# Kernel tuning notes

Hardware: AMD Instinct MI355X
Metric: run time of the kernel (lower is better)

The kernel has to match this reference:

```python
import jax, jax.numpy as jnp
import numpy as np
from jax import lax

B, C, H, W = 8, 1024, 64, 48
A = 9  # anchors per location

def _conv(x, w, b, pad):
    y = lax.conv_general_dilated(x, w, (1, 1), pad,
                                 dimension_numbers=('NCHW', 'OIHW', 'NCHW'))
    return y + b[None, :, None, None]

def setup_inputs() -> dict:
    key = jax.random.key(0)
    ks = jax.random.split(key, 12)
    base_feat = jax.random.normal(ks[0], (B, C, H, W), dtype=jnp.float32)
    W_conv = jax.random.normal(ks[1], (512, C, 3, 3), dtype=jnp.float32) * 0.01
    b_conv = jnp.zeros((512,), jnp.float32)
    W_cls = jax.random.normal(ks[2], (18, 512, 1, 1), dtype=jnp.float32) * 0.01
    b_cls = jnp.zeros((18,), jnp.float32)
    W_bbox = jax.random.normal(ks[3], (36, 512, 1, 1), dtype=jnp.float32) * 0.01
    b_bbox = jnp.zeros((36,), jnp.float32)
    # anchor-target-layer outputs (data-dependent assignment) provided as inputs
    rpn_label = (jax.random.randint(ks[4], (B, A * H * W), 0, 3) - 1).astype(jnp.int32)  # {-1,0,1}
    rpn_bbox_targets = jax.random.normal(ks[5], (B, 36, H, W), dtype=jnp.float32) * 0.1
    rpn_bbox_inside_weights = (jax.random.uniform(ks[6], (B, 36, H, W)) < 0.25).astype(jnp.float32)
    rpn_bbox_outside_weights = jax.random.uniform(ks[7], (B, 36, H, W), dtype=jnp.float32) * 0.01
    return {"base_feat": base_feat, "W_conv": W_conv, "b_conv": b_conv,
            "W_cls": W_cls, "b_cls": b_cls, "W_bbox": W_bbox, "b_bbox": b_bbox,
            "rpn_label": rpn_label, "rpn_bbox_targets": rpn_bbox_targets,
            "rpn_bbox_inside_weights": rpn_bbox_inside_weights,
            "rpn_bbox_outside_weights": rpn_bbox_outside_weights}

def reference(base_feat, W_conv, b_conv, W_cls, b_cls, W_bbox, b_bbox,
              rpn_label, rpn_bbox_targets, rpn_bbox_inside_weights,
              rpn_bbox_outside_weights):
    # RPN head: 3x3 conv + relu, then 1x1 cls / bbox heads
    rpn_conv1 = jax.nn.relu(_conv(base_feat, W_conv, b_conv, ((1, 1), (1, 1))))
    cls_score = _conv(rpn_conv1, W_cls, b_cls, ((0, 0), (0, 0)))   # [B,18,H,W]
    bbox_pred = _conv(rpn_conv1, W_bbox, b_bbox, ((0, 0), (0, 0)))  # [B,36,H,W]
    # reshape to [B,2,A*H,W], softmax over the 2-way fg/bg axis, reshape back
    score_rs = cls_score.reshape(B, 2, A * H, W)
    prob_rs = jax.nn.softmax(score_rs, axis=1)
    rpn_cls_prob = prob_rs.reshape(B, 18, H, W)
    # classification loss: permute(0,2,3,1).view(-1,2), keep labels != -1
    logits = score_rs.transpose(0, 2, 3, 1).reshape(-1, 2)
    label = rpn_label.reshape(-1)
    valid = (label != -1).astype(logits.dtype)
    logp = jax.nn.log_softmax(logits, axis=-1)
    lbl = jnp.clip(label, 0, 1)
    nll = -jnp.take_along_axis(logp, lbl[:, None].astype(jnp.int32), axis=1)[:, 0]
    rpn_loss_cls = jnp.sum(nll * valid) / jnp.maximum(jnp.sum(valid), 1.0)
    # smooth-L1 box loss, sigma=3, summed over dims [1,2,3], mean over batch
    sigma2 = 9.0
    in_diff = rpn_bbox_inside_weights * (bbox_pred - rpn_bbox_targets)
    abs_d = jnp.abs(in_diff)
    sign = lax.stop_gradient((abs_d < 1.0 / sigma2).astype(abs_d.dtype))
    in_loss = in_diff * in_diff * (sigma2 / 2.0) * sign + (abs_d - 0.5 / sigma2) * (1.0 - sign)
    rpn_loss_box = jnp.mean(jnp.sum(rpn_bbox_outside_weights * in_loss, axis=(1, 2, 3)))
    return rpn_cls_prob, bbox_pred, rpn_loss_cls, rpn_loss_box
```

## Files before the change

### kernel.cpp

```cpp
#include <hip/hip_runtime.h>
#include <stdint.h>

#define B_    8
#define CIN   1024
#define H_    64
#define W_    48
#define OC    512
#define HW    3072
#define NPOS  24576
#define K9    9216
#define HP    66
#define WP    50

typedef __attribute__((ext_vector_type(8))) __bf16 bf16x8;
typedef __attribute__((ext_vector_type(4))) float  float4_t;
typedef __attribute__((ext_vector_type(4))) unsigned short ushort4_t;
typedef __attribute__((ext_vector_type(8))) int int8v;
typedef __attribute__((ext_vector_type(4))) int int4v;

__device__ __forceinline__ unsigned short f2bf(float x) {
  union { float f; unsigned u; } v; v.f = x;
  unsigned r = v.u + 0x7FFFu + ((v.u >> 16) & 1u);
  return (unsigned short)(r >> 16);
}

__device__ __forceinline__ unsigned int pack4_fp8(float a, float b, float c, float d) {
  int w = __builtin_amdgcn_cvt_pk_fp8_f32(a, b, 0, false);
  w = __builtin_amdgcn_cvt_pk_fp8_f32(c, d, w, true);
  return (unsigned int)w;
}

__device__ __forceinline__ void async16(const void* g, void* l) {
  __builtin_amdgcn_global_load_lds(
      (const __attribute__((address_space(1))) unsigned int*)g,
      (__attribute__((address_space(3))) unsigned int*)l, 16, 0, 0);
}

__device__ __forceinline__ float wave_sum(float v) {
  for (int o = 32; o > 0; o >>= 1) v += __shfl_down(v, o, 64);
  return v;
}

__global__ void prep_fused(const float* __restrict__ x, const float* __restrict__ Wc,
                           const float* __restrict__ Wcls, const float* __restrict__ Wbb,
                           unsigned char* __restrict__ xt, unsigned char* __restrict__ Wa,
                           unsigned short* __restrict__ Wh, float* __restrict__ accbuf) {
  __shared__ float smem[9216];
  int bid = blockIdx.x, t = threadIdx.x;
  if (bid < 4096) {
    int cx = bid & 7, h = (bid >> 3) & 63, b = bid >> 9;
    float* tile = smem;
    const float* src = x + ((long)(b * CIN + cx * 128) * H_ + h) * W_;
    for (int it = 0; it < 6; ++it) {
      int e = it * 256 + t;
      int cl = e / 12, w4 = e % 12;
      float4_t v = *(const float4_t*)&src[(long)cl * HW + w4 * 4];
      int base = cl * 49 + w4 * 4;
      tile[base] = v.x; tile[base + 1] = v.y; tile[base + 2] = v.z; tile[base + 3] = v.w;
    }
    __syncthreads();
    unsigned char* dst = xt + ((long)(b * HP + h + 1) * WP + 1) * CIN + cx * 128;
    for (int it = 0; it < 6; ++it) {
      int e = it * 256 + t;
      int w = e >> 5, g = e & 31;
      float v0 = tile[(g * 4 + 0) * 49 + w] * 16.f;
      float v1 = tile[(g * 4 + 1) * 49 + w] * 16.f;
      float v2 = tile[(g * 4 + 2) * 49 + w] * 16.f;
      float v3 = tile[(g * 4 + 3) * 49 + w] * 16.f;
      *(unsigned int*)&dst[(long)w * CIN + g * 4] = pack4_fp8(v0, v1, v2, v3);
    }
  } else if (bid < 4608) {
    int o = bid - 4096;
    float* lw = smem;
    const float* src = Wc + (long)o * K9;
    for (int i = 0; i < 9; ++i)
      *(float4_t*)&lw[i * 1024 + t * 4] = *(const float4_t*)&src[i * 1024 + t * 4];
    __syncthreads();
    unsigned char* dst = Wa + (long)o * K9;
    int c = t * 4;
    for (int off = 0; off < 9; ++off) {
      float v0 = lw[(c + 0) * 9 + off] * 512.f;
      float v1 = lw[(c + 1) * 9 + off] * 512.f;
      float v2 = lw[(c + 2) * 9 + off] * 512.f;
      float v3 = lw[(c + 3) * 9 + off] * 512.f;
      *(unsigned int*)&dst[off * 1024 + c] = pack4_fp8(v0, v1, v2, v3);
    }
  } else if (bid < 4640) {
    int e = (bid - 4608) * 1024 + t * 4;
    int m = e >> 9, c = e & 511;
    float v0 = 0.f, v1 = 0.f, v2 = 0.f, v3 = 0.f;
    if (m < 18) {
      const float* s = Wcls + m * 512 + c;
      v0 = s[0]; v1 = s[1]; v2 = s[2]; v3 = s[3];
    } else if (m < 54) {
      const float* s = Wbb + (m - 18) * 512 + c;
      v0 = s[0]; v1 = s[1]; v2 = s[2]; v3 = s[3];
    }
    ushort4_t pk; pk.x = f2bf(v0); pk.y = f2bf(v1); pk.z = f2bf(v2); pk.w = f2bf(v3);
    *(ushort4_t*)&Wh[e] = pk;
    if (bid == 4608 && t < 4) accbuf[t] = 0.f;
  } else {
    int bid2 = bid - 4640;
    int b = bid2 / 66, h = bid2 % 66;
    unsigned char* base = xt + (long)(b * 66 + h) * 50 * 1024;
    int4v z = {};
    if (h == 0 || h == 65) {
      for (int i = t; i < 3200; i += 256) *(int4v*)(base + (long)i * 16) = z;
    } else if (t < 128) {
      int which = t >> 6, off = t & 63;
      *(int4v*)(base + (long)which * 49 * 1024 + (long)off * 16) = z;
    }
  }
}

__global__ __launch_bounds__(256, 2)
void conv_gemm(const unsigned char* __restrict__ Wa, const unsigned char* __restrict__ xt,
               const float* __restrict__ bias, unsigned short* __restrict__ conv1) {
  __shared__ unsigned char As_[128 * 128];
  __shared__ unsigned char Bs_[2][192 * 128];
  int t = threadIdx.x;
  int lane = t & 63, wv = t >> 6;
  int m0 = blockIdx.y * 128;
  int n0 = blockIdx.x * 192;
  const unsigned char* aSrc[4];
  const unsigned char* bSrc[6];
  for (int s = 0; s < 4; ++s) {
    int c = s * 256 + t;
    int r = c >> 3;
    int q = (c & 7) ^ (r & 7);
    aSrc[s] = Wa + (long)(m0 + r) * K9 + q * 16;
  }
  for (int p = 0; p < 6; ++p) {
    int c = p * 256 + t;
    int r = c >> 3;
    int q = (c & 7) ^ (r & 7);
    int n = n0 + r; int b = n / HW; int rem = n % HW; int h = rem / W_; int w = rem % W_;
    bSrc[p] = xt + ((long)(b * HP + h) * WP + w) * CIN + q * 16;
  }
  float4_t acc[4][6] = {};
  int wm = wv >> 1, wn = wv & 1;
  int quad = lane >> 4, col = lane & 15;

  auto stageA = [&](int kt) {
    long aoff = (long)kt * 128;
    for (int s = 0; s < 4; ++s)
      async16(aSrc[s] + aoff, &As_[s * 4096 + wv * 1024]);
  };
  auto stageB = [&](int buf, int kt) {
    int off = kt >> 3;
    int dy = off / 3, dx = off % 3;
    long boff = (long)(dy * WP + dx) * CIN + (kt & 7) * 128;
    for (int p = 0; p < 6; ++p)
      async16(bSrc[p] + boff, &Bs_[buf][p * 4096 + wv * 1024]);
  };

  stageA(0);
  stageB(0, 0);
#pragma unroll 1
  for (int kt = 0; kt < 72; ++kt) {
    if (kt + 1 < 72) {
      stageB((kt + 1) & 1, kt + 1);
      asm volatile("s_waitcnt vmcnt(6)\n\ts_barrier" ::: "memory");
    } else {
      asm volatile("s_waitcnt vmcnt(0)\n\ts_barrier" ::: "memory");
    }
    const unsigned char* Bcur = Bs_[kt & 1];
    int8v af[4], bfr[6];
    for (int i = 0; i < 4; ++i) {
      int r = wm * 64 + i * 16 + col;
      int rb = r * 128, x7 = r & 7;
      int4v lo = *(const int4v*)&As_[rb + (((quad * 2 + 0) ^ x7) << 4)];
      int4v hi = *(const int4v*)&As_[rb + (((quad * 2 + 1) ^ x7) << 4)];
      af[i] = (int8v){lo.x, lo.y, lo.z, lo.w, hi.x, hi.y, hi.z, hi.w};
    }
    for (int j = 0; j < 6; ++j) {
      int r = wn * 96 + j * 16 + col;
      int rb = r * 128, x7 = r & 7;
      int4v lo = *(const int4v*)&Bcur[rb + (((quad * 2 + 0) ^ x7) << 4)];
      int4v hi = *(const int4v*)&Bcur[rb + (((quad * 2 + 1) ^ x7) << 4)];
      bfr[j] = (int8v){lo.x, lo.y, lo.z, lo.w, hi.x, hi.y, hi.z, hi.w};
    }
    asm volatile("s_waitcnt lgkmcnt(0)\n\ts_barrier" ::: "memory");
    __builtin_amdgcn_sched_barrier(0);
    if (kt + 1 < 72) stageA(kt + 1);
    __builtin_amdgcn_sched_barrier(0);
    __builtin_amdgcn_s_setprio(1);
    for (int i = 0; i < 4; ++i)
      for (int j = 0; j < 6; ++j)
        acc[i][j] = __builtin_amdgcn_mfma_scale_f32_16x16x128_f8f6f4(
            af[i], bfr[j], acc[i][j], 0, 0, 0, 0x76767676, 0, 0x7B7B7B7B);
    __builtin_amdgcn_s_setprio(0);
    __builtin_amdgcn_sched_barrier(0);
  }

  for (int i = 0; i < 4; ++i) {
    int mb = m0 + wm * 64 + i * 16 + quad * 4;
    float b0 = bias[mb + 0], b1 = bias[mb + 1], b2 = bias[mb + 2], b3 = bias[mb + 3];
    for (int j = 0; j < 6; ++j) {
      int n = n0 + wn * 96 + j * 16 + col;
      ushort4_t pk;
      pk.x = f2bf(fmaxf(acc[i][j].x + b0, 0.f));
      pk.y = f2bf(fmaxf(acc[i][j].y + b1, 0.f));
      pk.z = f2bf(fmaxf(acc[i][j].z + b2, 0.f));
      pk.w = f2bf(fmaxf(acc[i][j].w + b3, 0.f));
      *(ushort4_t*)&conv1[(long)n * 512 + mb] = pk;
    }
  }
}

__global__ __launch_bounds__(256, 2)
void head_gemm(const unsigned short* __restrict__ Wh, const unsigned short* __restrict__ conv1,
               const float* __restrict__ b_cls, const float* __restrict__ b_bbox,
               float* __restrict__ cls_ws, float* __restrict__ out_bbox) {
  __shared__ unsigned short As[64 * 128];
  __shared__ unsigned short Bs[64 * 128];
  int t = threadIdx.x;
  int lane = t & 63, wv = t >> 6;
  int n0 = blockIdx.x * 64;
  int quad = lane >> 4, col = lane & 15;
  const unsigned short* aS[4];
  const unsigned short* bS[4];
  for (int p = 0; p < 4; ++p) {
    int c = p * 256 + t;
    int r = c >> 4;
    int q = (c & 15) ^ (r & 15);
    aS[p] = Wh + (long)r * 512 + q * 8;
    bS[p] = conv1 + (long)(n0 + r) * 512 + q * 8;
  }
  float4_t acc[4] = {};
  for (int kt = 0; kt < 4; ++kt) {
    long koff = (long)kt * 128;
    __syncthreads();
    for (int p = 0; p < 4; ++p) async16(aS[p] + koff, &As[p * 2048 + wv * 512]);
    for (int p = 0; p < 4; ++p) async16(bS[p] + koff, &Bs[p * 2048 + wv * 512]);
    __syncthreads();
    for (int ks = 0; ks < 4; ++ks) {
      int rn = wv * 16 + col;
      bf16x8 bfr = *(const bf16x8*)&Bs[rn * 128 + (((ks * 4 + quad) ^ (rn & 15)) << 3)];
      for (int i = 0; i < 4; ++i) {
        int r = i * 16 + col;
        bf16x8 af = *(const bf16x8*)&As[r * 128 + (((ks * 4 + quad) ^ (r & 15)) << 3)];
        acc[i] = __builtin_amdgcn_mfma_f32_16x16x32_bf16(af, bfr, acc[i], 0, 0, 0);
      }
    }
  }
  int n = n0 + wv * 16 + col;
  int b = n / HW; int rem = n % HW;
  for (int i = 0; i < 4; ++i) {
    for (int r = 0; r < 4; ++r) {
      int m = i * 16 + quad * 4 + r;
      float v = acc[i][r];
      if (m < 18) {
        cls_ws[(long)(b * 18 + m) * HW + rem] = v + b_cls[m];
      } else if (m < 54) {
        out_bbox[(long)(b * 36 + (m - 18)) * HW + rem] = v + b_bbox[m - 18];
      }
    }
  }
}

__global__ void loss_fused(const float* __restrict__ cls, const int* __restrict__ label,
                           float* __restrict__ prob,
                           const float* __restrict__ pred, const float* __restrict__ tgt,
                           const float* __restrict__ iw, const float* __restrict__ ow,
                           float* __restrict__ acc) {
  int lane = threadIdx.x & 63, wv = threadIdx.x >> 6;
  __shared__ float red[8];
  if (blockIdx.x < 864) {
    int idx = blockIdx.x * 256 + threadIdx.x;
    int b = idx / 27648; int r = idx % 27648;
    int a = r / HW; int r2 = r % HW;
    long i0 = (long)(b * 18 + a) * HW + r2;
    long i1 = i0 + (long)9 * HW;
    float x0 = cls[i0], x1 = cls[i1];
    float mx = fmaxf(x0, x1);
    float e0 = __expf(x0 - mx), e1 = __expf(x1 - mx);
    float s = e0 + e1;
    prob[i0] = e0 / s;
    prob[i1] = e1 / s;
    int lb = label[idx];
    float nll = 0.f, val = 0.f;
    if (lb != -1) {
      val = 1.f;
      float xl = (lb > 0) ? x1 : x0;
      nll = -(xl - mx - __logf(s));
    }
    nll = wave_sum(nll);
    val = wave_sum(val);
    if (lane == 0) { red[wv] = nll; red[4 + wv] = val; }
    __syncthreads();
    if (threadIdx.x == 0) {
      atomicAdd(&acc[0], red[0] + red[1] + red[2] + red[3]);
      atomicAdd(&acc[1], red[4] + red[5] + red[6] + red[7]);
    }
  } else {
    int bid = blockIdx.x - 864;
    float s = 0.f;
    const long total = (long)B_ * 36 * HW;
    for (long i = (long)bid * 256 + threadIdx.x; i < total; i += (long)1728 * 256) {
      float d = iw[i] * (pred[i] - tgt[i]);
      float ad = fabsf(d);
      float l = (ad < (1.f / 9.f)) ? d * d * 4.5f : ad - (1.f / 18.f);
      s += ow[i] * l;
    }
    s = wave_sum(s);
    if (lane == 0) red[wv] = s;
    __syncthreads();
    if (threadIdx.x == 0) atomicAdd(&acc[2], red[0] + red[1] + red[2] + red[3]);
  }
}

__global__ void finalize(const float* __restrict__ acc, float* __restrict__ out) {
  if (threadIdx.x == 0) {
    out[0] = acc[0] / fmaxf(acc[1], 1.f);
    out[1] = acc[2] / (float)B_;
  }
}

extern "C" void kernel_launch(void* const* d_in, const int* in_sizes, int n_in,
                              void* d_out, int out_size, void* d_ws, size_t ws_size,
                              hipStream_t stream) {
  const float* base_feat = (const float*)d_in[0];
  const float* W_conv    = (const float*)d_in[1];
  const float* b_conv    = (const float*)d_in[2];
  const float* W_cls     = (const float*)d_in[3];
  const float* b_cls     = (const float*)d_in[4];
  const float* W_bbox    = (const float*)d_in[5];
  const float* b_bbox    = (const float*)d_in[6];
  const int*   rpn_label = (const int*)d_in[7];
  const float* bb_tgt    = (const float*)d_in[8];
  const float* bb_iw     = (const float*)d_in[9];
  const float* bb_ow     = (const float*)d_in[10];

  float* out = (float*)d_out;
  float* out_cls_prob = out;
  float* out_bbox     = out + 442368;
  float* out_scalars  = out + 442368 + 884736;

  size_t off = 0;
  auto alloc = [&](size_t bytes) {
    void* p = (char*)d_ws + off;
    off = (off + bytes + 255) & ~(size_t)255;
    return p;
  };
  const size_t XT_BYTES = (size_t)B_ * HP * WP * CIN;
  unsigned char*  xt    = (unsigned char*)alloc(XT_BYTES);
  unsigned char*  Wa    = (unsigned char*)alloc((size_t)OC * K9);
  unsigned short* conv1 = (unsigned short*)alloc((size_t)NPOS * OC * 2);
  unsigned short* Wh    = (unsigned short*)alloc((size_t)64 * 512 * 2);
  float* cls_ws         = (float*)alloc((size_t)B_ * 18 * HW * 4);
  float* accbuf         = (float*)alloc(16);

  prep_fused<<<5168, 256, 0, stream>>>(base_feat, W_conv, W_cls, W_bbox, xt, Wa, Wh, accbuf);
  conv_gemm<<<dim3(128, 4), 256, 0, stream>>>(Wa, xt, b_conv, conv1);
  head_gemm<<<384, 256, 0, stream>>>(Wh, conv1, b_cls, b_bbox, cls_ws, out_bbox);
  loss_fused<<<2592, 256, 0, stream>>>(cls_ws, rpn_label, out_cls_prob,
                                       out_bbox, bb_tgt, bb_iw, bb_ow, accbuf);
  finalize<<<1, 64, 0, stream>>>(accbuf, out_scalars);
}
```

Measured before the change: 342.5 us.

## Load GEMM A-operand fragments directly from global into registers, dropping LDS staging

```diff
diff --git a/kernel.cpp b/kernel.cpp
--- a/kernel.cpp
+++ b/kernel.cpp
@@ -116,20 +116,14 @@
 __global__ __launch_bounds__(256, 2)
 void conv_gemm(const unsigned char* __restrict__ Wa, const unsigned char* __restrict__ xt,
                const float* __restrict__ bias, unsigned short* __restrict__ conv1) {
-  __shared__ unsigned char As_[128 * 128];
   __shared__ unsigned char Bs_[2][192 * 128];
   int t = threadIdx.x;
   int lane = t & 63, wv = t >> 6;
   int m0 = blockIdx.y * 128;
   int n0 = blockIdx.x * 192;
-  const unsigned char* aSrc[4];
+  int wm = wv >> 1, wn = wv & 1;
+  int quad = lane >> 4, col = lane & 15;
   const unsigned char* bSrc[6];
-  for (int s = 0; s < 4; ++s) {
-    int c = s * 256 + t;
-    int r = c >> 3;
-    int q = (c & 7) ^ (r & 7);
-    aSrc[s] = Wa + (long)(m0 + r) * K9 + q * 16;
-  }
   for (int p = 0; p < 6; ++p) {
     int c = p * 256 + t;
     int r = c >> 3;
@@ -137,15 +131,12 @@
     int n = n0 + r; int b = n / HW; int rem = n % HW; int h = rem / W_; int w = rem % W_;
     bSrc[p] = xt + ((long)(b * HP + h) * WP + w) * CIN + q * 16;
   }
+  const unsigned char* aBase[4];
+  for (int i = 0; i < 4; ++i)
+    aBase[i] = Wa + (long)(m0 + wm * 64 + i * 16 + col) * K9 + quad * 32;
+
   float4_t acc[4][6] = {};
-  int wm = wv >> 1, wn = wv & 1;
-  int quad = lane >> 4, col = lane & 15;
-
-  auto stageA = [&](int kt) {
-    long aoff = (long)kt * 128;
-    for (int s = 0; s < 4; ++s)
-      async16(aSrc[s] + aoff, &As_[s * 4096 + wv * 1024]);
-  };
+
   auto stageB = [&](int buf, int kt) {
     int off = kt >> 3;
     int dy = off / 3, dx = off % 3;
@@ -154,25 +145,26 @@
       async16(bSrc[p] + boff, &Bs_[buf][p * 4096 + wv * 1024]);
   };
 
-  stageA(0);
   stageB(0, 0);
+  __builtin_amdgcn_sched_barrier(0);
+  int4v aLo[4], aHi[4];
+  for (int i = 0; i < 4; ++i) {
+    aLo[i] = *(const int4v*)(aBase[i]);
+    aHi[i] = *(const int4v*)(aBase[i] + 16);
+  }
+  __builtin_amdgcn_sched_barrier(0);
+
 #pragma unroll 1
   for (int kt = 0; kt < 72; ++kt) {
     if (kt + 1 < 72) {
       stageB((kt + 1) & 1, kt + 1);
-      asm volatile("s_waitcnt vmcnt(6)\n\ts_barrier" ::: "memory");
+      asm volatile("s_waitcnt vmcnt(14)\n\ts_barrier" ::: "memory");
     } else {
-      asm volatile("s_waitcnt vmcnt(0)\n\ts_barrier" ::: "memory");
-    }
+      asm volatile("s_waitcnt vmcnt(8)\n\ts_barrier" ::: "memory");
+    }
+    __builtin_amdgcn_sched_barrier(0);
     const unsigned char* Bcur = Bs_[kt & 1];
-    int8v af[4], bfr[6];
-    for (int i = 0; i < 4; ++i) {
-      int r = wm * 64 + i * 16 + col;
-      int rb = r * 128, x7 = r & 7;
-      int4v lo = *(const int4v*)&As_[rb + (((quad * 2 + 0) ^ x7) << 4)];
-      int4v hi = *(const int4v*)&As_[rb + (((quad * 2 + 1) ^ x7) << 4)];
-      af[i] = (int8v){lo.x, lo.y, lo.z, lo.w, hi.x, hi.y, hi.z, hi.w};
-    }
+    int8v bfr[6];
     for (int j = 0; j < 6; ++j) {
       int r = wn * 96 + j * 16 + col;
       int rb = r * 128, x7 = r & 7;
@@ -182,7 +174,15 @@
     }
     asm volatile("s_waitcnt lgkmcnt(0)\n\ts_barrier" ::: "memory");
     __builtin_amdgcn_sched_barrier(0);
-    if (kt + 1 < 72) stageA(kt + 1);
+    int8v af[4];
+    for (int i = 0; i < 4; ++i)
+      af[i] = (int8v){aLo[i].x, aLo[i].y, aLo[i].z, aLo[i].w,
+                      aHi[i].x, aHi[i].y, aHi[i].z, aHi[i].w};
+    long ko = (kt + 1 < 72) ? (long)(kt + 1) * 128 : 0;
+    for (int i = 0; i < 4; ++i) {
+      aLo[i] = *(const int4v*)(aBase[i] + ko);
+      aHi[i] = *(const int4v*)(aBase[i] + ko + 16);
+    }
     __builtin_amdgcn_sched_barrier(0);
     __builtin_amdgcn_s_setprio(1);
     for (int i = 0; i < 4; ++i)
```

Result: slower. 408.1 us (+19.1%).

## Enlarge conv GEMM tile to 256x192 with 8 waves and interleaved A staging

Applied to the files above, without the earlier changes.

```diff
diff --git a/kernel.cpp b/kernel.cpp
--- a/kernel.cpp
+++ b/kernel.cpp
@@ -113,84 +113,125 @@
   }
 }
 
-__global__ __launch_bounds__(256, 2)
+__global__ __launch_bounds__(512, 2)
 void conv_gemm(const unsigned char* __restrict__ Wa, const unsigned char* __restrict__ xt,
                const float* __restrict__ bias, unsigned short* __restrict__ conv1) {
-  __shared__ unsigned char As_[128 * 128];
+  __shared__ unsigned char As_[2][256 * 128];
   __shared__ unsigned char Bs_[2][192 * 128];
   int t = threadIdx.x;
   int lane = t & 63, wv = t >> 6;
-  int m0 = blockIdx.y * 128;
+  int m0 = blockIdx.y * 256;
   int n0 = blockIdx.x * 192;
+  int wm = wv >> 1, wn = wv & 1;
+  int quad = lane >> 4, col = lane & 15;
+
   const unsigned char* aSrc[4];
-  const unsigned char* bSrc[6];
   for (int s = 0; s < 4; ++s) {
-    int c = s * 256 + t;
+    int c = s * 512 + t;
     int r = c >> 3;
     int q = (c & 7) ^ (r & 7);
     aSrc[s] = Wa + (long)(m0 + r) * K9 + q * 16;
   }
-  for (int p = 0; p < 6; ++p) {
-    int c = p * 256 + t;
+  const unsigned char* bSrc[3];
+  for (int p = 0; p < 3; ++p) {
+    int c = p * 512 + t;
     int r = c >> 3;
     int q = (c & 7) ^ (r & 7);
     int n = n0 + r; int b = n / HW; int rem = n % HW; int h = rem / W_; int w = rem % W_;
     bSrc[p] = xt + ((long)(b * HP + h) * WP + w) * CIN + q * 16;
   }
+
   float4_t acc[4][6] = {};
-  int wm = wv >> 1, wn = wv & 1;
-  int quad = lane >> 4, col = lane & 15;
-
-  auto stageA = [&](int kt) {
-    long aoff = (long)kt * 128;
-    for (int s = 0; s < 4; ++s)
-      async16(aSrc[s] + aoff, &As_[s * 4096 + wv * 1024]);
-  };
+
   auto stageB = [&](int buf, int kt) {
     int off = kt >> 3;
     int dy = off / 3, dx = off % 3;
     long boff = (long)(dy * WP + dx) * CIN + (kt & 7) * 128;
-    for (int p = 0; p < 6; ++p)
-      async16(bSrc[p] + boff, &Bs_[buf][p * 4096 + wv * 1024]);
+    for (int p = 0; p < 3; ++p)
+      async16(bSrc[p] + boff, &Bs_[buf][p * 8192 + t * 16]);
   };
-
-  stageA(0);
+  auto stageA2 = [&](int buf, int kt, int s0) {
+    long aoff = (long)kt * 128;
+    for (int s = s0; s < s0 + 2; ++s)
+      async16(aSrc[s] + aoff, &As_[buf][s * 8192 + t * 16]);
+  };
+
   stageB(0, 0);
+  stageA2(0, 0, 0);
+  stageA2(0, 0, 2);
+
 #pragma unroll 1
   for (int kt = 0; kt < 72; ++kt) {
-    if (kt + 1 < 72) {
-      stageB((kt + 1) & 1, kt + 1);
-      asm volatile("s_waitcnt vmcnt(6)\n\ts_barrier" ::: "memory");
+    int cur = kt & 1, nxt = cur ^ 1;
+    if (kt < 71) {
+      stageB(nxt, kt + 1);
+      asm volatile("s_waitcnt vmcnt(3)\n\ts_barrier" ::: "memory");
     } else {
       asm volatile("s_waitcnt vmcnt(0)\n\ts_barrier" ::: "memory");
     }
-    const unsigned char* Bcur = Bs_[kt & 1];
+    const unsigned char* A  = As_[cur];
+    const unsigned char* Bc = Bs_[cur];
     int8v af[4], bfr[6];
     for (int i = 0; i < 4; ++i) {
       int r = wm * 64 + i * 16 + col;
       int rb = r * 128, x7 = r & 7;
-      int4v lo = *(const int4v*)&As_[rb + (((quad * 2 + 0) ^ x7) << 4)];
-      int4v hi = *(const int4v*)&As_[rb + (((quad * 2 + 1) ^ x7) << 4)];
+      int4v lo = *(const int4v*)&A[rb + (((quad * 2 + 0) ^ x7) << 4)];
+      int4v hi = *(const int4v*)&A[rb + (((quad * 2 + 1) ^ x7) << 4)];
       af[i] = (int8v){lo.x, lo.y, lo.z, lo.w, hi.x, hi.y, hi.z, hi.w};
     }
-    for (int j = 0; j < 6; ++j) {
+    for (int j = 0; j < 2; ++j) {
       int r = wn * 96 + j * 16 + col;
       int rb = r * 128, x7 = r & 7;
-      int4v lo = *(const int4v*)&Bcur[rb + (((quad * 2 + 0) ^ x7) << 4)];
-      int4v hi = *(const int4v*)&Bcur[rb + (((quad * 2 + 1) ^ x7) << 4)];
+      int4v lo = *(const int4v*)&Bc[rb + (((quad * 2 + 0) ^ x7) << 4)];
+      int4v hi = *(const int4v*)&Bc[rb + (((quad * 2 + 1) ^ x7) << 4)];
       bfr[j] = (int8v){lo.x, lo.y, lo.z, lo.w, hi.x, hi.y, hi.z, hi.w};
     }
-    asm volatile("s_waitcnt lgkmcnt(0)\n\ts_barrier" ::: "memory");
-    __builtin_amdgcn_sched_barrier(0);
-    if (kt + 1 < 72) stageA(kt + 1);
+    if (kt < 71) stageA2(nxt, kt + 1, 0);
+    asm volatile("s_barrier" ::: "memory");
+    asm volatile("s_waitcnt lgkmcnt(0)" ::: "memory");
     __builtin_amdgcn_sched_barrier(0);
     __builtin_amdgcn_s_setprio(1);
     for (int i = 0; i < 4; ++i)
-      for (int j = 0; j < 6; ++j)
+      for (int j = 0; j < 2; ++j)
         acc[i][j] = __builtin_amdgcn_mfma_scale_f32_16x16x128_f8f6f4(
             af[i], bfr[j], acc[i][j], 0, 0, 0, 0x76767676, 0, 0x7B7B7B7B);
     __builtin_amdgcn_s_setprio(0);
+    asm volatile("s_barrier" ::: "memory");
+    for (int j = 2; j < 4; ++j) {
+      int r = wn * 96 + j * 16 + col;
+      int rb = r * 128, x7 = r & 7;
+      int4v lo = *(const int4v*)&Bc[rb + (((quad * 2 + 0) ^ x7) << 4)];
+      int4v hi = *(const int4v*)&Bc[rb + (((quad * 2 + 1) ^ x7) << 4)];
+      bfr[j] = (int8v){lo.x, lo.y, lo.z, lo.w, hi.x, hi.y, hi.z, hi.w};
+    }
+    if (kt < 71) stageA2(nxt, kt + 1, 2);
+    asm volatile("s_barrier" ::: "memory");
+    asm volatile("s_waitcnt lgkmcnt(0)" ::: "memory");
     __builtin_amdgcn_sched_barrier(0);
+    __builtin_amdgcn_s_setprio(1);
+    for (int i = 0; i < 4; ++i)
+      for (int j = 2; j < 4; ++j)
+        acc[i][j] = __builtin_amdgcn_mfma_scale_f32_16x16x128_f8f6f4(
+            af[i], bfr[j], acc[i][j], 0, 0, 0, 0x76767676, 0, 0x7B7B7B7B);
+    __builtin_amdgcn_s_setprio(0);
+    asm volatile("s_barrier" ::: "memory");
+    for (int j = 4; j < 6; ++j) {
+      int r = wn * 96 + j * 16 + col;
+      int rb = r * 128, x7 = r & 7;
+      int4v lo = *(const int4v*)&Bc[rb + (((quad * 2 + 0) ^ x7) << 4)];
+      int4v hi = *(const int4v*)&Bc[rb + (((quad * 2 + 1) ^ x7) << 4)];
+      bfr[j] = (int8v){lo.x, lo.y, lo.z, lo.w, hi.x, hi.y, hi.z, hi.w};
+    }
+    asm volatile("s_barrier" ::: "memory");
+    asm volatile("s_waitcnt lgkmcnt(0)" ::: "memory");
+    __builtin_amdgcn_sched_barrier(0);
+    __builtin_amdgcn_s_setprio(1);
+    for (int i = 0; i < 4; ++i)
+      for (int j = 4; j < 6; ++j)
+        acc[i][j] = __builtin_amdgcn_mfma_scale_f32_16x16x128_f8f6f4(
+            af[i], bfr[j], acc[i][j], 0, 0, 0, 0x76767676, 0, 0x7B7B7B7B);
+    __builtin_amdgcn_s_setprio(0);
+    asm volatile("s_barrier" ::: "memory");
   }
 
   for (int i = 0; i < 4; ++i) {
@@ -352,7 +393,7 @@
   float* accbuf         = (float*)alloc(16);
 
   prep_fused<<<5168, 256, 0, stream>>>(base_feat, W_conv, W_cls, W_bbox, xt, Wa, Wh, accbuf);
-  conv_gemm<<<dim3(128, 4), 256, 0, stream>>>(Wa, xt, b_conv, conv1);
+  conv_gemm<<<dim3(128, 2), 512, 0, stream>>>(Wa, xt, b_conv, conv1);
   head_gemm<<<384, 256, 0, stream>>>(Wh, conv1, b_cls, b_bbox, cls_ws, out_bbox);
   loss_fused<<<2592, 256, 0, stream>>>(cls_ws, rpn_label, out_cls_prob,
                                        out_bbox, bb_tgt, bb_iw, bb_ow, accbuf);
```

Measured after the change: 370.3 us. 8.1% more time.

## Stage a halo input tile per channel chunk and reuse it across all nine taps

Applied to the files above, without the earlier changes.

```diff
diff --git a/kernel.cpp b/kernel.cpp
--- a/kernel.cpp
+++ b/kernel.cpp
@@ -116,81 +116,99 @@
 __global__ __launch_bounds__(256, 2)
 void conv_gemm(const unsigned char* __restrict__ Wa, const unsigned char* __restrict__ xt,
                const float* __restrict__ bias, unsigned short* __restrict__ conv1) {
-  __shared__ unsigned char As_[128 * 128];
-  __shared__ unsigned char Bs_[2][192 * 128];
+  __shared__ unsigned char As_[2][128 * 128];
+  __shared__ unsigned char Bt[2560 * 16];
   int t = threadIdx.x;
   int lane = t & 63, wv = t >> 6;
   int m0 = blockIdx.y * 128;
   int n0 = blockIdx.x * 192;
+  int wm = wv >> 1, wn = wv & 1;
+  int quad = lane >> 4, col = lane & 15;
+  int bB = n0 / HW;
+  int h0 = (n0 % HW) / W_;
+
+  long bOff[10];
+  for (int i = 0; i < 10; ++i) {
+    int c = i * 256 + t;
+    int p = c >> 3, s = c & 7;
+    int pc = (p < 300) ? p : 0;
+    int q = s ^ (pc & 7);
+    int r = pc / 50, w = pc % 50;
+    bOff[i] = ((long)(bB * HP + h0 + r) * WP + w) * CIN + q * 16;
+  }
+  auto stageB = [&](int cc) {
+    long co = (long)cc * 128;
+    for (int i = 0; i < 10; ++i)
+      async16(xt + bOff[i] + co, &Bt[(i * 256 + wv * 64) * 16]);
+  };
+
   const unsigned char* aSrc[4];
-  const unsigned char* bSrc[6];
   for (int s = 0; s < 4; ++s) {
     int c = s * 256 + t;
     int r = c >> 3;
     int q = (c & 7) ^ (r & 7);
     aSrc[s] = Wa + (long)(m0 + r) * K9 + q * 16;
   }
-  for (int p = 0; p < 6; ++p) {
-    int c = p * 256 + t;
-    int r = c >> 3;
-    int q = (c & 7) ^ (r & 7);
-    int n = n0 + r; int b = n / HW; int rem = n % HW; int h = rem / W_; int w = rem % W_;
-    bSrc[p] = xt + ((long)(b * HP + h) * WP + w) * CIN + q * 16;
-  }
+  auto stageA = [&](int buf, int aoff) {
+    for (int s = 0; s < 4; ++s)
+      async16(aSrc[s] + aoff, &As_[buf][s * 4096 + wv * 1024]);
+  };
+
+  int pbase[6];
+  for (int j = 0; j < 6; ++j) {
+    int nl = wn * 96 + j * 16 + col;
+    int hl = nl / W_, wl = nl % W_;
+    pbase[j] = hl * 50 + wl;
+  }
+
   float4_t acc[4][6] = {};
-  int wm = wv >> 1, wn = wv & 1;
-  int quad = lane >> 4, col = lane & 15;
-
-  auto stageA = [&](int kt) {
-    long aoff = (long)kt * 128;
-    for (int s = 0; s < 4; ++s)
-      async16(aSrc[s] + aoff, &As_[s * 4096 + wv * 1024]);
-  };
-  auto stageB = [&](int buf, int kt) {
-    int off = kt >> 3;
-    int dy = off / 3, dx = off % 3;
-    long boff = (long)(dy * WP + dx) * CIN + (kt & 7) * 128;
-    for (int p = 0; p < 6; ++p)
-      async16(bSrc[p] + boff, &Bs_[buf][p * 4096 + wv * 1024]);
-  };
-
-  stageA(0);
-  stageB(0, 0);
+  int q2 = quad * 2;
+
+  stageB(0);
+  stageA(0, 0);
+  int abuf = 0;
+
 #pragma unroll 1
-  for (int kt = 0; kt < 72; ++kt) {
-    if (kt + 1 < 72) {
-      stageB((kt + 1) & 1, kt + 1);
-      asm volatile("s_waitcnt vmcnt(6)\n\ts_barrier" ::: "memory");
-    } else {
+  for (int cc = 0; cc < 8; ++cc) {
+#pragma unroll 1
+    for (int tap = 0; tap < 9; ++tap) {
       asm volatile("s_waitcnt vmcnt(0)\n\ts_barrier" ::: "memory");
-    }
-    const unsigned char* Bcur = Bs_[kt & 1];
-    int8v af[4], bfr[6];
-    for (int i = 0; i < 4; ++i) {
-      int r = wm * 64 + i * 16 + col;
-      int rb = r * 128, x7 = r & 7;
-      int4v lo = *(const int4v*)&As_[rb + (((quad * 2 + 0) ^ x7) << 4)];
-      int4v hi = *(const int4v*)&As_[rb + (((quad * 2 + 1) ^ x7) << 4)];
-      af[i] = (int8v){lo.x, lo.y, lo.z, lo.w, hi.x, hi.y, hi.z, hi.w};
-    }
-    for (int j = 0; j < 6; ++j) {
-      int r = wn * 96 + j * 16 + col;
-      int rb = r * 128, x7 = r & 7;
-      int4v lo = *(const int4v*)&Bcur[rb + (((quad * 2 + 0) ^ x7) << 4)];
-      int4v hi = *(const int4v*)&Bcur[rb + (((quad * 2 + 1) ^ x7) << 4)];
-      bfr[j] = (int8v){lo.x, lo.y, lo.z, lo.w, hi.x, hi.y, hi.z, hi.w};
-    }
-    asm volatile("s_waitcnt lgkmcnt(0)\n\ts_barrier" ::: "memory");
-    __builtin_amdgcn_sched_barrier(0);
-    if (kt + 1 < 72) stageA(kt + 1);
-    __builtin_amdgcn_sched_barrier(0);
-    __builtin_amdgcn_s_setprio(1);
-    for (int i = 0; i < 4; ++i)
-      for (int j = 0; j < 6; ++j)
-        acc[i][j] = __builtin_amdgcn_mfma_scale_f32_16x16x128_f8f6f4(
-            af[i], bfr[j], acc[i][j], 0, 0, 0, 0x76767676, 0, 0x7B7B7B7B);
-    __builtin_amdgcn_s_setprio(0);
-    __builtin_amdgcn_sched_barrier(0);
+      const unsigned char* A = As_[abuf];
+      int dy = tap / 3, dx = tap - dy * 3;
+      int doff = dy * 50 + dx;
+      int8v af[4], bfr[6];
+      for (int i = 0; i < 4; ++i) {
+        int r = wm * 64 + i * 16 + col;
+        int rb = r * 128, x7 = r & 7;
+        int4v lo = *(const int4v*)&A[rb + (((q2 + 0) ^ x7) << 4)];
+        int4v hi = *(const int4v*)&A[rb + (((q2 + 1) ^ x7) << 4)];
+        af[i] = (int8v){lo.x, lo.y, lo.z, lo.w, hi.x, hi.y, hi.z, hi.w};
+      }
+      for (int j = 0; j < 6; ++j) {
+        int pj = pbase[j] + doff;
+        int rb = pj << 7, x7 = pj & 7;
+        int4v lo = *(const int4v*)&Bt[rb + (((q2 + 0) ^ x7) << 4)];
+        int4v hi = *(const int4v*)&Bt[rb + (((q2 + 1) ^ x7) << 4)];
+        bfr[j] = (int8v){lo.x, lo.y, lo.z, lo.w, hi.x, hi.y, hi.z, hi.w};
+      }
+      asm volatile("s_waitcnt lgkmcnt(0)\n\ts_barrier" ::: "memory");
+      __builtin_amdgcn_sched_barrier(0);
+      int nt = tap + 1, ncc = cc;
+      if (nt == 9) { nt = 0; ++ncc; }
+      if (ncc < 8) {
+        stageA(abuf ^ 1, nt * 1024 + ncc * 128);
+        if (nt == 0) stageB(ncc);
+      }
+      __builtin_amdgcn_sched_barrier(0);
+      __builtin_amdgcn_s_setprio(1);
+      for (int i = 0; i < 4; ++i)
+        for (int j = 0; j < 6; ++j)
+          acc[i][j] = __builtin_amdgcn_mfma_scale_f32_16x16x128_f8f6f4(
+              af[i], bfr[j], acc[i][j], 0, 0, 0, 0x76767676, 0, 0x7B7B7B7B);
+      __builtin_amdgcn_s_setprio(0);
+      __builtin_amdgcn_sched_barrier(0);
+      abuf ^= 1;
+    }
   }
 
   for (int i = 0; i < 4; ++i) {
```

Result: faster. 333.2 us (-2.7%).
